# Performance work log

Measured on AMD Instinct MI355X. Metric: run time of the kernel, lower is better.

The kernel has to match this reference:

```python
import jax, jax.numpy as jnp
import numpy as np

D_MODEL = 512
N_HEADS = 8
D_HEAD = D_MODEL // N_HEADS


def entmax15(z, axis=-1):
    """Exact sort-based entmax-1.5 along `axis` (Peters et al. 2019)."""
    z = jnp.moveaxis(z, axis, -1)
    x = z / 2.0
    x = x - jnp.max(x, axis=-1, keepdims=True)
    x_srt = -jnp.sort(-x, axis=-1)  # descending
    D = x_srt.shape[-1]
    k = jnp.arange(1, D + 1, dtype=x.dtype)
    cs = jnp.cumsum(x_srt, axis=-1)
    cs2 = jnp.cumsum(x_srt * x_srt, axis=-1)
    mean = cs / k
    ss = k * (cs2 / k - mean * mean)
    delta = (1.0 - ss) / k
    tau = mean - jnp.sqrt(jnp.clip(delta, 0.0))
    support = (tau <= x_srt).astype(jnp.int32)
    support_size = jnp.sum(support, axis=-1, keepdims=True)  # >= 1
    tau_star = jnp.take_along_axis(tau, support_size - 1, axis=-1)
    out = jnp.square(jnp.clip(x - tau_star, 0.0))
    return jnp.moveaxis(out, -1, axis)


def setup_inputs() -> dict:
    key = jax.random.key(0)
    ks = jax.random.split(key, 12)
    B, L = 8, 1024
    s = 1.0 / np.sqrt(D_MODEL)
    inp = {
        "query": jax.random.normal(ks[0], (B, L, D_MODEL), jnp.float32),
        "key": jax.random.normal(ks[1], (B, L, D_MODEL), jnp.float32),
        "value": jax.random.normal(ks[2], (B, L, D_MODEL), jnp.float32),
        "key_padding_mask": jnp.zeros((B, L), jnp.bool_),
        "q_w": jax.random.uniform(ks[3], (D_MODEL, D_MODEL), jnp.float32, -s, s),
        "q_b": jax.random.uniform(ks[4], (D_MODEL,), jnp.float32, -s, s),
        "k_w": jax.random.uniform(ks[5], (D_MODEL, D_MODEL), jnp.float32, -s, s),
        "k_b": jax.random.uniform(ks[6], (D_MODEL,), jnp.float32, -s, s),
        "v_w": jax.random.uniform(ks[7], (D_MODEL, D_MODEL), jnp.float32, -s, s),
        "v_b": jax.random.uniform(ks[8], (D_MODEL,), jnp.float32, -s, s),
        "out_w": jax.random.uniform(ks[9], (D_MODEL, D_MODEL), jnp.float32, -s, s),
        "out_b": jax.random.uniform(ks[10], (D_MODEL,), jnp.float32, -s, s),
    }
    return inp


def reference(query, key, value, key_padding_mask, q_w, q_b, k_w, k_b, v_w, v_b, out_w, out_b):
    B, L, _ = query.shape
    scale = D_HEAD ** -0.5
    # torch Linear: y = x @ W^T + b
    def split_heads(x):
        return x.reshape(B, L, N_HEADS, D_HEAD).transpose(0, 2, 1, 3)  # [B,H,L,d]
    q = split_heads(query @ q_w.T + q_b)
    k = split_heads(key @ k_w.T + k_b)
    v = split_heads(value @ v_w.T + v_b)
    scores = jnp.einsum('bhqd,bhkd->bhqk', q, k) * scale  # [B,H,L,L]
    mask = key_padding_mask[:, None, None, :]
    scores = jnp.where(mask, jnp.asarray(-1e9, scores.dtype), scores)
    attn = entmax15(scores, axis=-1)  # dropout in eval mode -> identity
    ctx = jnp.einsum('bhqk,bhkd->bhqd', attn, v)
    ctx = ctx.transpose(0, 2, 1, 3).reshape(B, L, D_MODEL)
    return ctx @ out_w.T + out_b
```

## Files before the change

### kernel.cpp

```cpp
#include <hip/hip_runtime.h>
#include <stdint.h>

typedef _Float16 f16;
typedef __attribute__((ext_vector_type(8))) f16 f16x8;
typedef __attribute__((ext_vector_type(2))) f16 h2;
typedef __attribute__((ext_vector_type(4))) float f32x4;
typedef unsigned short u16;
typedef unsigned int u32;
typedef unsigned char u8;

#define LL 1024
#define DM 512

__device__ __forceinline__ u16 f2h(float f){ return __builtin_bit_cast(u16, (f16)f); }
__device__ __forceinline__ u32 pack2(float a, float b){
  h2 v; v.x = (f16)a; v.y = (f16)b; return __builtin_bit_cast(u32, v);
}
__device__ __forceinline__ f32x4 mfma16h(f16x8 a, f16x8 b, f32x4 c){
  return __builtin_amdgcn_mfma_f32_16x16x32_f16(a, b, c, 0, 0, 0);
}

template<int CTRL>
__device__ __forceinline__ float dpp_mov(float x){
  return __builtin_bit_cast(float,
    __builtin_amdgcn_update_dpp(0, __builtin_bit_cast(int, x), CTRL, 0xF, 0xF, true));
}
__device__ __forceinline__ float red_add16(float v){
  v += dpp_mov<0x128>(v);
  v += dpp_mov<0x124>(v);
  v += dpp_mov<0x122>(v);
  v += dpp_mov<0x121>(v);
  return v;
}
__device__ __forceinline__ float red_max16(float v){
  v = fmaxf(v, dpp_mov<0x128>(v));
  v = fmaxf(v, dpp_mov<0x124>(v));
  v = fmaxf(v, dpp_mov<0x122>(v));
  v = fmaxf(v, dpp_mov<0x121>(v));
  return v;
}

struct CvtArgs {
  const float* src[7];
  u16* dst[7];
  int n4[7];
};

__global__ __launch_bounds__(256) void cvt_kernel(CvtArgs a){
  int seg = blockIdx.y;
  const float4* s = (const float4*)a.src[seg];
  ushort4* d = (ushort4*)a.dst[seg];
  int n4 = a.n4[seg];
  for (int i = blockIdx.x*blockDim.x + threadIdx.x; i < n4; i += gridDim.x*blockDim.x){
    float4 v = s[i];
    ushort4 o;
    o.x = f2h(v.x); o.y = f2h(v.y); o.z = f2h(v.z); o.w = f2h(v.w);
    d[i] = o;
  }
}

struct QkvArgs {
  const u16* A[3];
  const u16* W[3];
  const float* bias[3];
  u16* dst[3];
  float scale[3];
};

__global__ __launch_bounds__(256,2) void proj_qkv(QkvArgs args){
  __shared__ u16 SM[128*128];
  u16* As = SM;
  u16* Bs = SM + 128*64;
  const int tid = threadIdx.x;
  const int w = tid>>6, lane = tid&63;
  const int g = lane>>4, r16 = lane&15;
  const int wr = w>>1, wc = w&1;

  const int which = blockIdx.y>>2, nt = blockIdx.y&3;
  const bool isV = (which==2);
  const u16* A = args.A[which];
  const u16* W = args.W[which];
  const float* bias = args.bias[which];
  u16* dsth = args.dst[which];
  const float scale = args.scale[which];

  const int m0 = blockIdx.x*128, n0 = nt*128;

  f32x4 acc[4][4] = {};

  int rowc[4], slc[4];
  #pragma unroll
  for (int i=0;i<4;++i){
    int c = i*256+tid;
    rowc[i] = c>>3;
    slc[i] = (c&7) ^ ((c>>3)&7);
  }

  const int fswz = r16 & 7;

  for (int k0=0; k0<DM; k0+=64){
    #pragma unroll
    for (int i=0;i<4;++i){
      int c = i*256+tid;
      __builtin_amdgcn_global_load_lds(
        (const __attribute__((address_space(1))) void*)(A + (size_t)(m0+rowc[i])*DM + k0 + slc[i]*8),
        (__attribute__((address_space(3))) void*)(&As[c*8]), 16, 0, 0);
      __builtin_amdgcn_global_load_lds(
        (const __attribute__((address_space(1))) void*)(W + (size_t)(n0+rowc[i])*DM + k0 + slc[i]*8),
        (__attribute__((address_space(3))) void*)(&Bs[c*8]), 16, 0, 0);
    }
    __syncthreads();

    f16x8 af[4][2], bfr[4][2];
    #pragma unroll
    for (int mi=0; mi<4; ++mi){
      int row = wr*64 + mi*16 + r16;
      #pragma unroll
      for (int ks=0; ks<2; ++ks)
        af[mi][ks] = *(const f16x8*)(&As[row*64 + ((ks*4+g)^fswz)*8]);
    }
    #pragma unroll
    for (int ni=0; ni<4; ++ni){
      int row = wc*64 + ni*16 + r16;
      #pragma unroll
      for (int ks=0; ks<2; ++ks)
        bfr[ni][ks] = *(const f16x8*)(&Bs[row*64 + ((ks*4+g)^fswz)*8]);
    }
    if (isV){
      #pragma unroll
      for (int mi=0; mi<4; ++mi)
        #pragma unroll
        for (int ni=0; ni<4; ++ni){
          acc[mi][ni] = mfma16h(af[mi][0], bfr[ni][0], acc[mi][ni]);
          acc[mi][ni] = mfma16h(af[mi][1], bfr[ni][1], acc[mi][ni]);
        }
    } else {
      #pragma unroll
      for (int mi=0; mi<4; ++mi)
        #pragma unroll
        for (int ni=0; ni<4; ++ni){
          acc[mi][ni] = mfma16h(bfr[ni][0], af[mi][0], acc[mi][ni]);
          acc[mi][ni] = mfma16h(bfr[ni][1], af[mi][1], acc[mi][ni]);
        }
    }
    __syncthreads();
  }

  if (!isV){
    #pragma unroll
    for (int mi=0; mi<4; ++mi){
      #pragma unroll
      for (int ni=0; ni<4; ++ni){
        f32x4 a = acc[mi][ni];
        int row = wr*64 + mi*16 + r16;
        int c   = wc*16 + ni*4 + g;
        float4 bv = *(const float4*)(bias + n0 + c*4);
        uint2 pk;
        pk.x = pack2((a[0]+bv.x)*scale, (a[1]+bv.y)*scale);
        pk.y = pack2((a[2]+bv.z)*scale, (a[3]+bv.w)*scale);
        *(uint2*)(&SM[row*128 + ((c ^ ((row&7)<<2))<<2)]) = pk;
      }
    }
  } else {
    #pragma unroll
    for (int mi=0; mi<4; ++mi){
      #pragma unroll
      for (int ni=0; ni<4; ++ni){
        f32x4 a = acc[mi][ni];
        int fl = wc*64 + ni*16 + r16;
        int kc = wr*16 + mi*4 + g;
        float bv = bias[n0 + fl];
        uint2 pk;
        pk.x = pack2(a[0]+bv, a[1]+bv);
        pk.y = pack2(a[2]+bv, a[3]+bv);
        *(uint2*)(&SM[fl*128 + ((kc ^ ((fl&7)<<2))<<2)]) = pk;
      }
    }
  }
  __syncthreads();

  #pragma unroll
  for (int rr=0; rr<8; ++rr){
    int row = w*32 + rr*4 + (lane>>4);
    int c0 = (lane&15)*2;
    int cs = c0 ^ ((row&7)<<2);
    uint4 v = *(const uint4*)(&SM[row*128 + (cs<<2)]);
    if (!isV){
      *(uint4*)(dsth + (size_t)(m0+row)*DM + n0 + (c0<<2)) = v;
    } else {
      int n = n0 + row;
      int hh = n>>6, d = n&63, bb = m0>>10;
      *(uint4*)(dsth + (size_t)((bb*8+hh)*64 + d)*1024 + (m0&1023) + (c0<<2)) = v;
    }
  }
}

__global__ __launch_bounds__(256,2) void proj_out(
    const u16* __restrict__ A, const u16* __restrict__ W,
    const float* __restrict__ bias, float* __restrict__ dstf)
{
  __shared__ u16 As[64*64];
  __shared__ u16 Bs[128*64];
  const int tid = threadIdx.x;
  const int w = tid>>6, lane = tid&63;
  const int g = lane>>4, r16 = lane&15;
  const int m0 = blockIdx.x*64, n0 = blockIdx.y*128;

  f32x4 acc[4][2] = {};

  int rowa[2], slota[2];
  #pragma unroll
  for (int i=0;i<2;++i){ int c = i*256+tid; rowa[i]=c>>3; slota[i]=c&7; }
  int rowb[4], slotb[4];
  #pragma unroll
  for (int i=0;i<4;++i){ int c = i*256+tid; rowb[i]=c>>3; slotb[i]=c&7; }

  uint4 ra[2], rb[4];
  #pragma unroll
  for (int i=0;i<2;++i)
    ra[i] = *(const uint4*)(A + (size_t)(m0+rowa[i])*DM + slota[i]*8);
  #pragma unroll
  for (int i=0;i<4;++i)
    rb[i] = *(const uint4*)(W + (size_t)(n0+rowb[i])*DM + slotb[i]*8);

  const int fswz = r16 & 7;

  for (int k0=0; k0<DM; k0+=64){
    __syncthreads();
    #pragma unroll
    for (int i=0;i<2;++i)
      *(uint4*)(&As[rowa[i]*64 + (slota[i]^(rowa[i]&7))*8]) = ra[i];
    #pragma unroll
    for (int i=0;i<4;++i)
      *(uint4*)(&Bs[rowb[i]*64 + (slotb[i]^(rowb[i]&7))*8]) = rb[i];
    __syncthreads();
    int kn = (k0+64 < DM) ? (k0+64) : 0;
    #pragma unroll
    for (int i=0;i<2;++i)
      ra[i] = *(const uint4*)(A + (size_t)(m0+rowa[i])*DM + kn + slota[i]*8);
    #pragma unroll
    for (int i=0;i<4;++i)
      rb[i] = *(const uint4*)(W + (size_t)(n0+rowb[i])*DM + kn + slotb[i]*8);

    f16x8 af[4][2], bfr[2][2];
    #pragma unroll
    for (int mi=0; mi<4; ++mi){
      int row = mi*16 + r16;
      #pragma unroll
      for (int ks=0; ks<2; ++ks)
        af[mi][ks] = *(const f16x8*)(&As[row*64 + ((ks*4+g)^fswz)*8]);
    }
    #pragma unroll
    for (int ni=0; ni<2; ++ni){
      int row = w*32 + ni*16 + r16;
      #pragma unroll
      for (int ks=0; ks<2; ++ks)
        bfr[ni][ks] = *(const f16x8*)(&Bs[row*64 + ((ks*4+g)^fswz)*8]);
    }
    #pragma unroll
    for (int mi=0; mi<4; ++mi)
      #pragma unroll
      for (int ni=0; ni<2; ++ni){
        acc[mi][ni] = mfma16h(bfr[ni][0], af[mi][0], acc[mi][ni]);
        acc[mi][ni] = mfma16h(bfr[ni][1], af[mi][1], acc[mi][ni]);
      }
  }

  #pragma unroll
  for (int mi=0; mi<4; ++mi){
    #pragma unroll
    for (int ni=0; ni<2; ++ni){
      int m  = m0 + mi*16 + r16;
      int nb = n0 + w*32 + ni*16 + g*4;
      float4 bv = *(const float4*)(bias + nb);
      float4 o;
      o.x = acc[mi][ni][0]+bv.x; o.y = acc[mi][ni][1]+bv.y;
      o.z = acc[mi][ni][2]+bv.z; o.w = acc[mi][ni][3]+bv.w;
      *(float4*)(dstf + (size_t)m*DM + nb) = o;
    }
  }
}

__global__ __launch_bounds__(512,4) void attn_entmax(
    const u16* __restrict__ Qf, const u16* __restrict__ Kf,
    const u16* __restrict__ Vt, const u8* __restrict__ mask,
    u16* __restrict__ ctx)
{
  __shared__ u16 S[32*1024];

  const int tid = threadIdx.x, w = tid>>6, lane = tid&63;
  const int g = lane>>4, r16 = lane&15;
  const int bid = blockIdx.x;
  const int bh = ((bid&7)<<3) | ((bid>>3)&7);
  const int qb = bid>>6;
  const int b = bh>>3, h = bh&7;
  const int q0 = qb*32;
  const u16* Qb = Qf + ((size_t)(b*LL + q0))*DM + h*64;
  const u16* Kb = Kf + ((size_t)(b*LL))*DM + h*64;

  f16x8 qf[2][2];
  #pragma unroll
  for (int qi=0;qi<2;++qi){
    qf[qi][0] = *(const f16x8*)(Qb + (size_t)(qi*16 + r16)*DM + g*8);
    qf[qi][1] = *(const f16x8*)(Qb + (size_t)(qi*16 + r16)*DM + 32 + g*8);
  }
  {
    f16x8 kc[2][2], kn[2][2];
    #pragma unroll
    for (int j=0;j<2;++j){
      const u16* kp = Kb + (size_t)(w*128 + j*16 + r16)*DM + g*8;
      kc[j][0] = *(const f16x8*)(kp);
      kc[j][1] = *(const f16x8*)(kp + 32);
    }
    #pragma unroll
    for (int grp=0; grp<4; ++grp){
      #pragma unroll
      for (int j=0;j<2;++j){
        if (grp < 3){
          const u16* kp = Kb + (size_t)(w*128 + (grp*2+2+j)*16 + r16)*DM + g*8;
          kn[j][0] = *(const f16x8*)(kp);
          kn[j][1] = *(const f16x8*)(kp + 32);
        }
      }
      #pragma unroll
      for (int j=0;j<2;++j){
        int kt = grp*2 + j;
        int krow = w*128 + kt*16;
        int kb = krow + g*4;
        u32 m4 = *(const u32*)(mask + b*LL + kb);
        #pragma unroll
        for (int qi=0; qi<2; ++qi){
          f32x4 acc = {};
          acc = mfma16h(kc[j][0], qf[qi][0], acc);
          acc = mfma16h(kc[j][1], qf[qi][1], acc);
          float v0 = (m4 & 0xFFu)       ? -30000.f : acc[0];
          float v1 = (m4 & 0xFF00u)     ? -30000.f : acc[1];
          float v2 = (m4 & 0xFF0000u)   ? -30000.f : acc[2];
          float v3 = (m4 & 0xFF000000u) ? -30000.f : acc[3];
          int row = qi*16 + r16;
          int cc = ((kb>>6)&7) ^ (row&7);
          uint2 pk; pk.x = pack2(v0,v1); pk.y = pack2(v2,v3);
          *(uint2*)(&S[row*LL + (kb ^ (cc<<3))]) = pk;
        }
      }
      #pragma unroll
      for (int j=0;j<2;++j){ kc[j][0]=kn[j][0]; kc[j][1]=kn[j][1]; }
    }
  }
  __syncthreads();

  {
    const int r = w*4 + g;
    const int ccb = (r16 ^ r) & 7;
    h2 zp[32];
    #pragma unroll
    for (int c=0;c<8;++c){
      uint4 v = *(const uint4*)(&S[r*LL + ((r16*64 + c*8) ^ (ccb<<3))]);
      zp[c*4+0] = __builtin_bit_cast(h2, v.x);
      zp[c*4+1] = __builtin_bit_cast(h2, v.y);
      zp[c*4+2] = __builtin_bit_cast(h2, v.z);
      zp[c*4+3] = __builtin_bit_cast(h2, v.w);
    }
    h2 m2 = zp[0];
    #pragma unroll
    for (int t=1;t<32;++t) m2 = __builtin_elementwise_max(m2, zp[t]);
    float mx = red_max16(fmaxf((float)m2.x, (float)m2.y));

    const h2 zero2 = (h2)(f16)0;
    float lo = mx - 1.0f, hi = mx, tau = mx - 0.5f;
    #pragma unroll 1
    for (int it=0; it<6; ++it){
      f16 th = (f16)tau;
      h2 t2; t2.x = th; t2.y = th;
      h2 s1a = zero2, s1b = zero2, s2a = zero2, s2b = zero2;
      #pragma unroll
      for (int t=0;t<32;t+=2){
        h2 d0 = __builtin_elementwise_max(zp[t]   - t2, zero2);
        h2 d1 = __builtin_elementwise_max(zp[t+1] - t2, zero2);
        s1a = s1a + d0;        s1b = s1b + d1;
        s2a = s2a + d0*d0;     s2b = s2b + d1*d1;
      }
      h2 s1h = s1a + s1b, s2h = s2a + s2b;
      float s1 = red_add16((float)s1h.x + (float)s1h.y);
      float s2 = red_add16((float)s2h.x + (float)s2h.y);
      if (s2 >= 1.0f) lo = tau; else hi = tau;
      float tn = tau + (s2 - 1.0f)/(2.0f*s1);
      tau = (tn >= lo && tn < hi) ? tn : 0.5f*(lo+hi);
    }

    {
      f16 th = (f16)tau;
      h2 t2; t2.x = th; t2.y = th;
      h2 psa = zero2, psb = zero2;
      #pragma unroll
      for (int t=0;t<32;t+=2){
        h2 d0 = __builtin_elementwise_max(zp[t]   - t2, zero2);
        h2 d1 = __builtin_elementwise_max(zp[t+1] - t2, zero2);
        h2 p0 = d0*d0, p1 = d1*d1;
        zp[t] = p0; zp[t+1] = p1;
        psa = psa + p0; psb = psb + p1;
      }
      h2 ps2 = psa + psb;
      float ps = red_add16((float)ps2.x + (float)ps2.y);
      f16 iv = (f16)(1.0f/ps);
      h2 i2; i2.x = iv; i2.y = iv;
      #pragma unroll
      for (int c=0;c<8;++c){
        uint4 v;
        v.x = __builtin_bit_cast(u32, (h2)(zp[c*4+0]*i2));
        v.y = __builtin_bit_cast(u32, (h2)(zp[c*4+1]*i2));
        v.z = __builtin_bit_cast(u32, (h2)(zp[c*4+2]*i2));
        v.w = __builtin_bit_cast(u32, (h2)(zp[c*4+3]*i2));
        *(uint4*)(&S[r*LL + ((r16*64 + c*8) ^ (ccb<<3))]) = v;
      }
    }
  }
  __syncthreads();

  const int qi = w>>2, di = w&3;
  const u16* vrow = Vt + (size_t)(bh*64 + di*16 + r16)*LL;
  const int prow = qi*16 + r16;
  f32x4 o0 = {}, o1 = {};
  {
    f16x8 pc[4], vc[4], pn[4], vn[4];
    #pragma unroll
    for (int j=0;j<4;++j){
      int k = j*32 + g*8;
      int cc = ((k>>6)&7) ^ (prow&7);
      pc[j] = *(const f16x8*)(&S[prow*LL + (k ^ (cc<<3))]);
      vc[j] = *(const f16x8*)(vrow + k);
    }
    #pragma unroll
    for (int grp=0; grp<8; ++grp){
      #pragma unroll
      for (int j=0;j<4;++j){
        if (grp < 7){
          int k = (grp*4+4+j)*32 + g*8;
          int cc = ((k>>6)&7) ^ (prow&7);
          pn[j] = *(const f16x8*)(&S[prow*LL + (k ^ (cc<<3))]);
          vn[j] = *(const f16x8*)(vrow + k);
        }
      }
      #pragma unroll
      for (int j=0;j<4;++j){
        if (j & 1) o1 = mfma16h(pc[j], vc[j], o1);
        else       o0 = mfma16h(pc[j], vc[j], o0);
      }
      #pragma unroll
      for (int j=0;j<4;++j){ pc[j]=pn[j]; vc[j]=vn[j]; }
    }
  }
  #pragma unroll
  for (int r=0;r<4;++r){
    int q = q0 + qi*16 + g*4 + r;
    ctx[(size_t)(b*LL + q)*DM + h*64 + di*16 + r16] = f2h(o0[r] + o1[r]);
  }
}

extern "C" void kernel_launch(void* const* d_in, const int* in_sizes, int n_in,
                              void* d_out, int out_size, void* d_ws, size_t ws_size,
                              hipStream_t stream) {
  const float* query = (const float*)d_in[0];
  const float* key   = (const float*)d_in[1];
  const float* value = (const float*)d_in[2];
  const u8*    maskp = (const u8*)d_in[3];
  const float* q_w = (const float*)d_in[4];
  const float* q_b = (const float*)d_in[5];
  const float* k_w = (const float*)d_in[6];
  const float* k_b = (const float*)d_in[7];
  const float* v_w = (const float*)d_in[8];
  const float* v_b = (const float*)d_in[9];
  const float* out_w = (const float*)d_in[10];
  const float* out_b = (const float*)d_in[11];
  float* out = (float*)d_out;

  u16* qx = (u16*)d_ws;
  u16* kx = qx + 4194304;
  u16* vx = kx + 4194304;
  u16* wq = vx + 4194304;
  u16* wk = wq + 262144;
  u16* wv = wk + 262144;
  u16* wo = wv + 262144;
  u16* Qbuf = wo + 262144;
  u16* Kbuf = Qbuf + 4194304;
  u16* Vt   = Kbuf + 4194304;
  u16* ctxb = Vt + 4194304;

  CvtArgs ca;
  ca.src[0]=query; ca.dst[0]=qx; ca.n4[0]=8*LL*DM/4;
  ca.src[1]=key;   ca.dst[1]=kx; ca.n4[1]=8*LL*DM/4;
  ca.src[2]=value; ca.dst[2]=vx; ca.n4[2]=8*LL*DM/4;
  ca.src[3]=q_w;   ca.dst[3]=wq; ca.n4[3]=DM*DM/4;
  ca.src[4]=k_w;   ca.dst[4]=wk; ca.n4[4]=DM*DM/4;
  ca.src[5]=v_w;   ca.dst[5]=wv; ca.n4[5]=DM*DM/4;
  ca.src[6]=out_w; ca.dst[6]=wo; ca.n4[6]=DM*DM/4;
  cvt_kernel<<<dim3(512,7),256,0,stream>>>(ca);

  QkvArgs qa;
  qa.A[0]=qx; qa.A[1]=kx; qa.A[2]=vx;
  qa.W[0]=wq; qa.W[1]=wk; qa.W[2]=wv;
  qa.bias[0]=q_b; qa.bias[1]=k_b; qa.bias[2]=v_b;
  qa.dst[0]=Qbuf; qa.dst[1]=Kbuf; qa.dst[2]=Vt;
  qa.scale[0]=0.0625f; qa.scale[1]=1.0f; qa.scale[2]=1.0f;

  proj_qkv<<<dim3(64,12),256,0,stream>>>(qa);

  attn_entmax<<<dim3(2048),512,0,stream>>>(Qbuf, Kbuf, Vt, maskp, ctxb);

  proj_out<<<dim3(128,4),256,0,stream>>>(ctxb, wo, out_b, out);
}
```

Baseline: 181.6 us.

## Double attention block threads to 1024 with split-K PV and LDS reduction

The attention block grows from 8 to 16 waves. Each wave now computes 64 keys of QK^T, each entmax row is split across 32 lanes instead of 16 (reductions extended with a cross-half shuffle), and the PV product is split over two key halves that are combined through a new float LDS buffer. This spreads per-block work thinly to raise latency hiding and cut per-thread register use. It adds an extra barrier and LDS traffic, and the larger blocks with more shared memory may limit how many blocks fit per CU.

```diff
diff --git a/kernel.cpp b/kernel.cpp
--- a/kernel.cpp
+++ b/kernel.cpp
@@ -37,6 +37,16 @@
   v = fmaxf(v, dpp_mov<0x124>(v));
   v = fmaxf(v, dpp_mov<0x122>(v));
   v = fmaxf(v, dpp_mov<0x121>(v));
+  return v;
+}
+__device__ __forceinline__ float red_add32(float v){
+  v = red_add16(v);
+  v += __shfl_xor(v, 16);
+  return v;
+}
+__device__ __forceinline__ float red_max32(float v){
+  v = red_max16(v);
+  v = fmaxf(v, __shfl_xor(v, 16));
   return v;
 }
 
@@ -281,12 +291,13 @@
   }
 }
 
-__global__ __launch_bounds__(512,4) void attn_entmax(
+__global__ __launch_bounds__(1024,8) void attn_entmax(
     const u16* __restrict__ Qf, const u16* __restrict__ Kf,
     const u16* __restrict__ Vt, const u8* __restrict__ mask,
     u16* __restrict__ ctx)
 {
   __shared__ u16 S[32*1024];
+  __shared__ float P2[2048];
 
   const int tid = threadIdx.x, w = tid>>6, lane = tid&63;
   const int g = lane>>4, r16 = lane&15;
@@ -305,57 +316,51 @@
     qf[qi][1] = *(const f16x8*)(Qb + (size_t)(qi*16 + r16)*DM + 32 + g*8);
   }
   {
-    f16x8 kc[2][2], kn[2][2];
-    #pragma unroll
-    for (int j=0;j<2;++j){
-      const u16* kp = Kb + (size_t)(w*128 + j*16 + r16)*DM + g*8;
-      kc[j][0] = *(const f16x8*)(kp);
-      kc[j][1] = *(const f16x8*)(kp + 32);
-    }
-    #pragma unroll
-    for (int grp=0; grp<4; ++grp){
-      #pragma unroll
-      for (int j=0;j<2;++j){
-        if (grp < 3){
-          const u16* kp = Kb + (size_t)(w*128 + (grp*2+2+j)*16 + r16)*DM + g*8;
-          kn[j][0] = *(const f16x8*)(kp);
-          kn[j][1] = *(const f16x8*)(kp + 32);
-        }
-      }
-      #pragma unroll
-      for (int j=0;j<2;++j){
-        int kt = grp*2 + j;
-        int krow = w*128 + kt*16;
-        int kb = krow + g*4;
-        u32 m4 = *(const u32*)(mask + b*LL + kb);
-        #pragma unroll
-        for (int qi=0; qi<2; ++qi){
-          f32x4 acc = {};
-          acc = mfma16h(kc[j][0], qf[qi][0], acc);
-          acc = mfma16h(kc[j][1], qf[qi][1], acc);
-          float v0 = (m4 & 0xFFu)       ? -30000.f : acc[0];
-          float v1 = (m4 & 0xFF00u)     ? -30000.f : acc[1];
-          float v2 = (m4 & 0xFF0000u)   ? -30000.f : acc[2];
-          float v3 = (m4 & 0xFF000000u) ? -30000.f : acc[3];
-          int row = qi*16 + r16;
-          int cc = ((kb>>6)&7) ^ (row&7);
-          uint2 pk; pk.x = pack2(v0,v1); pk.y = pack2(v2,v3);
-          *(uint2*)(&S[row*LL + (kb ^ (cc<<3))]) = pk;
-        }
-      }
-      #pragma unroll
-      for (int j=0;j<2;++j){ kc[j][0]=kn[j][0]; kc[j][1]=kn[j][1]; }
+    f16x8 kc0, kc1, kn0, kn1;
+    {
+      const u16* kp = Kb + (size_t)(w*64 + r16)*DM + g*8;
+      kc0 = *(const f16x8*)(kp);
+      kc1 = *(const f16x8*)(kp + 32);
+    }
+    #pragma unroll
+    for (int kt=0; kt<4; ++kt){
+      if (kt < 3){
+        const u16* kp = Kb + (size_t)(w*64 + (kt+1)*16 + r16)*DM + g*8;
+        kn0 = *(const f16x8*)(kp);
+        kn1 = *(const f16x8*)(kp + 32);
+      }
+      int kb = w*64 + kt*16 + g*4;
+      u32 m4 = *(const u32*)(mask + b*LL + kb);
+      #pragma unroll
+      for (int qi=0; qi<2; ++qi){
+        f32x4 acc = {};
+        acc = mfma16h(kc0, qf[qi][0], acc);
+        acc = mfma16h(kc1, qf[qi][1], acc);
+        float v0 = (m4 & 0xFFu)       ? -30000.f : acc[0];
+        float v1 = (m4 & 0xFF00u)     ? -30000.f : acc[1];
+        float v2 = (m4 & 0xFF0000u)   ? -30000.f : acc[2];
+        float v3 = (m4 & 0xFF000000u) ? -30000.f : acc[3];
+        int row = qi*16 + r16;
+        int cc = ((kb>>6)&7) ^ (row&7);
+        uint2 pk; pk.x = pack2(v0,v1); pk.y = pack2(v2,v3);
+        *(uint2*)(&S[row*LL + (kb ^ (cc<<3))]) = pk;
+      }
+      kc0 = kn0; kc1 = kn1;
     }
   }
   __syncthreads();
 
   {
-    const int r = w*4 + g;
-    const int ccb = (r16 ^ r) & 7;
-    h2 zp[32];
-    #pragma unroll
-    for (int c=0;c<8;++c){
-      uint4 v = *(const uint4*)(&S[r*LL + ((r16*64 + c*8) ^ (ccb<<3))]);
+    const int row = w*2 + (lane>>5);
+    const int l32 = lane&31;
+    int offs[4];
+    h2 zp[16];
+    #pragma unroll
+    for (int c=0;c<4;++c){
+      int kb = l32*32 + c*8;
+      int cc = ((kb>>6)&7) ^ (row&7);
+      offs[c] = row*LL + (kb ^ (cc<<3));
+      uint4 v = *(const uint4*)(&S[offs[c]]);
       zp[c*4+0] = __builtin_bit_cast(h2, v.x);
       zp[c*4+1] = __builtin_bit_cast(h2, v.y);
       zp[c*4+2] = __builtin_bit_cast(h2, v.z);
@@ -363,8 +368,8 @@
     }
     h2 m2 = zp[0];
     #pragma unroll
-    for (int t=1;t<32;++t) m2 = __builtin_elementwise_max(m2, zp[t]);
-    float mx = red_max16(fmaxf((float)m2.x, (float)m2.y));
+    for (int t=1;t<16;++t) m2 = __builtin_elementwise_max(m2, zp[t]);
+    float mx = red_max32(fmaxf((float)m2.x, (float)m2.y));
 
     const h2 zero2 = (h2)(f16)0;
     float lo = mx - 1.0f, hi = mx, tau = mx - 0.5f;
@@ -374,15 +379,15 @@
       h2 t2; t2.x = th; t2.y = th;
       h2 s1a = zero2, s1b = zero2, s2a = zero2, s2b = zero2;
       #pragma unroll
-      for (int t=0;t<32;t+=2){
+      for (int t=0;t<16;t+=2){
         h2 d0 = __builtin_elementwise_max(zp[t]   - t2, zero2);
         h2 d1 = __builtin_elementwise_max(zp[t+1] - t2, zero2);
         s1a = s1a + d0;        s1b = s1b + d1;
         s2a = s2a + d0*d0;     s2b = s2b + d1*d1;
       }
       h2 s1h = s1a + s1b, s2h = s2a + s2b;
-      float s1 = red_add16((float)s1h.x + (float)s1h.y);
-      float s2 = red_add16((float)s2h.x + (float)s2h.y);
+      float s1 = red_add32((float)s1h.x + (float)s1h.y);
+      float s2 = red_add32((float)s2h.x + (float)s2h.y);
       if (s2 >= 1.0f) lo = tau; else hi = tau;
       float tn = tau + (s2 - 1.0f)/(2.0f*s1);
       tau = (tn >= lo && tn < hi) ? tn : 0.5f*(lo+hi);
@@ -393,7 +398,7 @@
       h2 t2; t2.x = th; t2.y = th;
       h2 psa = zero2, psb = zero2;
       #pragma unroll
-      for (int t=0;t<32;t+=2){
+      for (int t=0;t<16;t+=2){
         h2 d0 = __builtin_elementwise_max(zp[t]   - t2, zero2);
         h2 d1 = __builtin_elementwise_max(zp[t+1] - t2, zero2);
         h2 p0 = d0*d0, p1 = d1*d1;
@@ -401,59 +406,70 @@
         psa = psa + p0; psb = psb + p1;
       }
       h2 ps2 = psa + psb;
-      float ps = red_add16((float)ps2.x + (float)ps2.y);
+      float ps = red_add32((float)ps2.x + (float)ps2.y);
       f16 iv = (f16)(1.0f/ps);
       h2 i2; i2.x = iv; i2.y = iv;
       #pragma unroll
-      for (int c=0;c<8;++c){
+      for (int c=0;c<4;++c){
         uint4 v;
         v.x = __builtin_bit_cast(u32, (h2)(zp[c*4+0]*i2));
         v.y = __builtin_bit_cast(u32, (h2)(zp[c*4+1]*i2));
         v.z = __builtin_bit_cast(u32, (h2)(zp[c*4+2]*i2));
         v.w = __builtin_bit_cast(u32, (h2)(zp[c*4+3]*i2));
-        *(uint4*)(&S[r*LL + ((r16*64 + c*8) ^ (ccb<<3))]) = v;
+        *(uint4*)(&S[offs[c]]) = v;
       }
     }
   }
   __syncthreads();
 
-  const int qi = w>>2, di = w&3;
+  const int qi = w>>3, di = (w>>1)&3, kh = w&1;
   const u16* vrow = Vt + (size_t)(bh*64 + di*16 + r16)*LL;
   const int prow = qi*16 + r16;
   f32x4 o0 = {}, o1 = {};
   {
-    f16x8 pc[4], vc[4], pn[4], vn[4];
-    #pragma unroll
-    for (int j=0;j<4;++j){
-      int k = j*32 + g*8;
-      int cc = ((k>>6)&7) ^ (prow&7);
-      pc[j] = *(const f16x8*)(&S[prow*LL + (k ^ (cc<<3))]);
-      vc[j] = *(const f16x8*)(vrow + k);
+    f16x8 pc0, pc1, vc0, vc1, pn0, pn1, vn0, vn1;
+    const int base = kh*16;
+    {
+      int k0c = (base+0)*32 + g*8;
+      int k1c = (base+1)*32 + g*8;
+      int cc0 = ((k0c>>6)&7) ^ (prow&7);
+      int cc1 = ((k1c>>6)&7) ^ (prow&7);
+      pc0 = *(const f16x8*)(&S[prow*LL + (k0c ^ (cc0<<3))]);
+      vc0 = *(const f16x8*)(vrow + k0c);
+      pc1 = *(const f16x8*)(&S[prow*LL + (k1c ^ (cc1<<3))]);
+      vc1 = *(const f16x8*)(vrow + k1c);
     }
     #pragma unroll
     for (int grp=0; grp<8; ++grp){
-      #pragma unroll
-      for (int j=0;j<4;++j){
-        if (grp < 7){
-          int k = (grp*4+4+j)*32 + g*8;
-          int cc = ((k>>6)&7) ^ (prow&7);
-          pn[j] = *(const f16x8*)(&S[prow*LL + (k ^ (cc<<3))]);
-          vn[j] = *(const f16x8*)(vrow + k);
-        }
-      }
-      #pragma unroll
-      for (int j=0;j<4;++j){
-        if (j & 1) o1 = mfma16h(pc[j], vc[j], o1);
-        else       o0 = mfma16h(pc[j], vc[j], o0);
-      }
-      #pragma unroll
-      for (int j=0;j<4;++j){ pc[j]=pn[j]; vc[j]=vn[j]; }
-    }
-  }
-  #pragma unroll
-  for (int r=0;r<4;++r){
-    int q = q0 + qi*16 + g*4 + r;
-    ctx[(size_t)(b*LL + q)*DM + h*64 + di*16 + r16] = f2h(o0[r] + o1[r]);
+      if (grp < 7){
+        int k0n = (base+grp*2+2)*32 + g*8;
+        int k1n = (base+grp*2+3)*32 + g*8;
+        int cc0 = ((k0n>>6)&7) ^ (prow&7);
+        int cc1 = ((k1n>>6)&7) ^ (prow&7);
+        pn0 = *(const f16x8*)(&S[prow*LL + (k0n ^ (cc0<<3))]);
+        vn0 = *(const f16x8*)(vrow + k0n);
+        pn1 = *(const f16x8*)(&S[prow*LL + (k1n ^ (cc1<<3))]);
+        vn1 = *(const f16x8*)(vrow + k1n);
+      }
+      o0 = mfma16h(pc0, vc0, o0);
+      o1 = mfma16h(pc1, vc1, o1);
+      pc0 = pn0; vc0 = vn0; pc1 = pn1; vc1 = vn1;
+    }
+  }
+  const int pair = qi*4 + di;
+  if (kh == 1){
+    float4 o;
+    o.x = o0[0]+o1[0]; o.y = o0[1]+o1[1]; o.z = o0[2]+o1[2]; o.w = o0[3]+o1[3];
+    *(float4*)(&P2[pair*256 + r16*16 + g*4]) = o;
+  }
+  __syncthreads();
+  if (kh == 0){
+    float4 p = *(const float4*)(&P2[pair*256 + r16*16 + g*4]);
+    u16* cp = ctx + (size_t)(b*LL + q0 + qi*16 + g*4)*DM + h*64 + di*16 + r16;
+    cp[0*DM] = f2h(o0[0]+o1[0]+p.x);
+    cp[1*DM] = f2h(o0[1]+o1[1]+p.y);
+    cp[2*DM] = f2h(o0[2]+o1[2]+p.z);
+    cp[3*DM] = f2h(o0[3]+o1[3]+p.w);
   }
 }
 
@@ -505,7 +521,7 @@
 
   proj_qkv<<<dim3(64,12),256,0,stream>>>(qa);
 
-  attn_entmax<<<dim3(2048),512,0,stream>>>(Qbuf, Kbuf, Vt, maskp, ctxb);
+  attn_entmax<<<dim3(2048),1024,0,stream>>>(Qbuf, Kbuf, Vt, maskp, ctxb);
 
   proj_out<<<dim3(128,4),256,0,stream>>>(ctxb, wo, out_b, out);
 }
```

Result: slower. 186.2 us (+2.6%).
